# Kernel optimization log

Measured on AMD Instinct MI355X. Metric: run time of the kernel, lower is better.

The kernel has to match this reference:

```python
import jax, jax.numpy as jnp
import numpy as np

BS, L, IMG, RS = 512, 68, 224, 7
R2 = RS * RS
DEPTH_SCALE = 500.0
VALID_RANGE = 90.0
THR = 1e-4


def setup_inputs() -> dict:
    key = jax.random.key(0)
    k1, k2, k3 = jax.random.split(key, 3)
    rel_depth_pred = jax.random.normal(k1, (BS, L, L), dtype=jnp.float32)
    depth = jax.random.uniform(k2, (BS, 1, IMG, IMG), dtype=jnp.float32)
    # landmarks in pixel coords well inside the 224px image so regions are valid
    landmarks = jax.random.uniform(k3, (BS, L, 2), dtype=jnp.float32) * 180.0 + 22.0
    scale_factor = jnp.ones((BS, 2), dtype=jnp.float32)
    bbox = jnp.zeros((BS, 4), dtype=jnp.float32)
    return {"rel_depth_pred": rel_depth_pred, "depth": depth,
            "landmarks": landmarks, "scale_factor": scale_factor, "bbox": bbox}


def _extract_landmark_depth(depth, landmarks, scale_factor, bbox):
    bs, img = depth.shape[0], depth.shape[3]
    # normalized landmark coords in [-1, 1]
    face_lm = (landmarks - bbox[:, None, :2]) * scale_factor[:, None, :] / img * 2.0 - 1.0  # [bs,L,2]
    x = jnp.linspace(-RS / 2.0, RS / 2.0, RS) / img * 2.0
    A, B = jnp.meshgrid(x, x, indexing='ij')          # A[i,j]=x[i], B[i,j]=x[j]
    offsets = jnp.stack([B, A], axis=2)               # torch: stack(meshgrid([x,x])[::-1], dim=2)
    grid = face_lm[:, :, None, None, :] + offsets     # [bs,L,RS,RS,2]
    grid = grid.reshape(bs, L * R2, 2)
    # F.grid_sample mode='nearest', padding='zeros', align_corners=False
    ix = ((grid[..., 0] + 1.0) * img - 1.0) * 0.5
    iy = ((grid[..., 1] + 1.0) * img - 1.0) * 0.5
    xi = jnp.round(ix).astype(jnp.int32)
    yi = jnp.round(iy).astype(jnp.int32)
    valid = (xi >= 0) & (xi < img) & (yi >= 0) & (yi < img)
    xi = jnp.clip(xi, 0, img - 1)
    yi = jnp.clip(yi, 0, img - 1)
    flat = depth.reshape(bs, img * img)
    vals = jnp.take_along_axis(flat, yi * img + xi, axis=1) * valid.astype(depth.dtype)
    regions = vals.reshape(bs, L, R2)
    s = jnp.sort(regions, axis=2)                     # ascending per landmark region
    m = s > THR
    m = m.at[:, :, 0].set(False)                      # torch zeroes index 0 before the diff
    trans = m[:, :, 1:] & ~m[:, :, :-1]               # single 0->1 transition (m is monotone)
    has = jnp.any(trans, axis=2)
    st = jnp.where(has, jnp.argmax(trans, axis=2) + 1, R2 - 1)  # fallback: last index
    med_ind = (st + R2 - 1) // 2                      # ((st + 48)/2).long()
    median = jnp.take_along_axis(s, med_ind[..., None], axis=2)[..., 0]  # [bs,L]
    # torch.median over dim=1: lower median = (L-1)//2-th order statistic
    med_of_med = jnp.sort(median, axis=1)[:, (L - 1) // 2]
    median_mask = jnp.abs(median - med_of_med[:, None]) < VALID_RANGE / DEPTH_SCALE
    return median, median_mask


def reference(rel_depth_pred, depth, landmarks, scale_factor, bbox):
    median, median_mask = _extract_landmark_depth(depth, landmarks, scale_factor, bbox)
    median = median * DEPTH_SCALE
    median_diff = median[:, :, None] - median[:, None, :]            # [bs,L,L]
    fm = median_mask.astype(rel_depth_pred.dtype)
    median_rel_mask = fm[:, :, None] * fm[:, None, :]                # [bs,L,L]
    d = rel_depth_pred - median_diff
    ad = jnp.abs(d)
    loss_ele = jnp.where(ad < 1.0, 0.5 * d * d, ad - 0.5)            # smooth_l1, reduction='none'
    loss = jnp.sum(loss_ele * median_rel_mask) / (jnp.sum(median_rel_mask) + 1e-4)
    return loss, median_diff, median_rel_mask
```

## Files before the change

### kernel.cpp

```cpp
#include <hip/hip_runtime.h>
#include <cfloat>

static constexpr int kBS  = 512;
static constexpr int kL   = 68;
static constexpr int kIMG = 224;
static constexpr int kR2  = 49;
static constexpr int kLL  = kL * kL;
static constexpr int kOutBlk = 256;
static constexpr int kNbx = (kLL + kOutBlk - 1) / kOutBlk;
static constexpr int kNPart = kNbx * kBS;

__device__ __forceinline__ float lin_off(int k) {
  float x;
  if (k == 6) {
    x = 3.5f;
  } else {
    float step = __fdiv_rn((float)k, 6.0f);
    float a = __fmul_rn(-3.5f, __fsub_rn(1.0f, step));
    float b = __fmul_rn(3.5f, step);
    x = __fadd_rn(a, b);
  }
  return __fmul_rn(__fdiv_rn(x, 224.0f), 2.0f);
}

__global__ __launch_bounds__(256) void k_median(
    const float* __restrict__ depth, const float* __restrict__ lmk,
    const float* __restrict__ scale, const float* __restrict__ bbox,
    float* __restrict__ med) {
  int wave = blockIdx.x * 4 + (threadIdx.x >> 6);
  int lane = threadIdx.x & 63;
  if (wave >= kBS * kL) return;
  int b = wave / kL;

  float lmx = lmk[wave * 2 + 0];
  float lmy = lmk[wave * 2 + 1];
  float sx = scale[b * 2 + 0], sy = scale[b * 2 + 1];
  float bx = bbox[b * 4 + 0],  by = bbox[b * 4 + 1];

  float tx = __fsub_rn(lmx, bx);
  tx = __fmul_rn(tx, sx);
  tx = __fdiv_rn(tx, 224.0f);
  tx = __fmul_rn(tx, 2.0f);
  float flmx = __fsub_rn(tx, 1.0f);
  float ty = __fsub_rn(lmy, by);
  ty = __fmul_rn(ty, sy);
  ty = __fdiv_rn(ty, 224.0f);
  ty = __fmul_rn(ty, 2.0f);
  float flmy = __fsub_rn(ty, 1.0f);

  float v = FLT_MAX;
  if (lane < kR2) {
    int i = lane / 7, j = lane - i * 7;
    float gx = __fadd_rn(flmx, lin_off(j));
    float gy = __fadd_rn(flmy, lin_off(i));
    float ix = __fmul_rn(__fsub_rn(__fmul_rn(__fadd_rn(gx, 1.0f), 224.0f), 1.0f), 0.5f);
    float iy = __fmul_rn(__fsub_rn(__fmul_rn(__fadd_rn(gy, 1.0f), 224.0f), 1.0f), 0.5f);
    int xi = (int)rintf(ix);
    int yi = (int)rintf(iy);
    bool valid = (xi >= 0) && (xi < kIMG) && (yi >= 0) && (yi < kIMG);
    int xc = min(max(xi, 0), kIMG - 1);
    int yc = min(max(yi, 0), kIMG - 1);
    float dv = depth[(size_t)b * (kIMG * kIMG) + yc * kIMG + xc];
    v = valid ? dv : 0.0f;
  }

  int cnt = 0, rank = 0;
  for (int j = 0; j < kR2; ++j) {
    float vj = __shfl(v, j, 64);
    cnt += (vj <= 1e-4f) ? 1 : 0;
    rank += ((vj < v) || (vj == v && j < lane)) ? 1 : 0;
  }
  int st = min(max(cnt, 1), kR2 - 1);
  int k = (st + kR2 - 1) >> 1;
  unsigned long long sel = __ballot(lane < kR2 && rank == k);
  int src = __ffsll(sel) - 1;
  float m = __shfl(v, src, 64);
  if (lane == 0) med[wave] = m;
}

__global__ __launch_bounds__(128) void k_mask(
    const float* __restrict__ med, float* __restrict__ m500,
    float* __restrict__ fm) {
  __shared__ float s[kL];
  __shared__ float mom_s;
  int b = blockIdx.x;
  int t = threadIdx.x;
  if (t < kL) s[t] = med[b * kL + t];
  __syncthreads();
  if (t < kL) {
    float v = s[t];
    int rank = 0;
    for (int j = 0; j < kL; ++j) {
      float vj = s[j];
      rank += ((vj < v) || (vj == v && j < t)) ? 1 : 0;
    }
    if (rank == (kL - 1) / 2) mom_s = v;
  }
  __syncthreads();
  if (t < kL) {
    float v = s[t];
    float diff = fabsf(__fsub_rn(v, mom_s));
    fm[b * kL + t] = (diff < 0.18f) ? 1.0f : 0.0f;
    m500[b * kL + t] = __fmul_rn(v, 500.0f);
  }
}

__global__ __launch_bounds__(256) void k_out(
    const float* __restrict__ rdp, const float* __restrict__ m500,
    const float* __restrict__ fm, float* __restrict__ out_diff,
    float* __restrict__ out_mask, double* __restrict__ part) {
  int b = blockIdx.y;
  int t = blockIdx.x * blockDim.x + threadIdx.x;
  double pn = 0.0, pd = 0.0;
  if (t < kLL) {
    int i = t / kL, j = t - i * kL;
    float mi = m500[b * kL + i];
    float mj = m500[b * kL + j];
    float diff = __fsub_rn(mi, mj);
    float mv = __fmul_rn(fm[b * kL + i], fm[b * kL + j]);
    size_t idx = (size_t)b * kLL + t;
    out_diff[idx] = diff;
    out_mask[idx] = mv;
    float d = __fsub_rn(rdp[idx], diff);
    float ad = fabsf(d);
    float le = (ad < 1.0f) ? __fmul_rn(__fmul_rn(0.5f, d), d)
                           : __fsub_rn(ad, 0.5f);
    pn = (double)__fmul_rn(le, mv);
    pd = (double)mv;
  }
  for (int off = 32; off > 0; off >>= 1) {
    pn += __shfl_down(pn, off, 64);
    pd += __shfl_down(pd, off, 64);
  }
  __shared__ double sn[4], sd[4];
  int w = threadIdx.x >> 6;
  if ((threadIdx.x & 63) == 0) { sn[w] = pn; sd[w] = pd; }
  __syncthreads();
  if (threadIdx.x == 0) {
    double tn = sn[0] + sn[1] + sn[2] + sn[3];
    double td = sd[0] + sd[1] + sd[2] + sd[3];
    int pb = blockIdx.y * gridDim.x + blockIdx.x;
    part[2 * pb + 0] = tn;
    part[2 * pb + 1] = td;
  }
}

__global__ __launch_bounds__(256) void k_final(
    const double* __restrict__ part, float* __restrict__ out0) {
  double pn = 0.0, pd = 0.0;
  for (int i = threadIdx.x; i < kNPart; i += 256) {
    pn += part[2 * i + 0];
    pd += part[2 * i + 1];
  }
  for (int off = 32; off > 0; off >>= 1) {
    pn += __shfl_down(pn, off, 64);
    pd += __shfl_down(pd, off, 64);
  }
  __shared__ double sn[4], sd[4];
  int w = threadIdx.x >> 6;
  if ((threadIdx.x & 63) == 0) { sn[w] = pn; sd[w] = pd; }
  __syncthreads();
  if (threadIdx.x == 0) {
    double tn = sn[0] + sn[1] + sn[2] + sn[3];
    double td = sd[0] + sd[1] + sd[2] + sd[3];
    out0[0] = (float)(tn / (td + 1e-4));
  }
}

extern "C" void kernel_launch(void* const* d_in, const int* in_sizes, int n_in,
                              void* d_out, int out_size, void* d_ws, size_t ws_size,
                              hipStream_t stream) {
  const float* rdp   = (const float*)d_in[0];
  const float* depth = (const float*)d_in[1];
  const float* lmk   = (const float*)d_in[2];
  const float* scale = (const float*)d_in[3];
  const float* bbox  = (const float*)d_in[4];

  float* out = (float*)d_out;
  float* out_diff = out + 1;
  float* out_mask = out + 1 + (size_t)kBS * kLL;

  char* ws = (char*)d_ws;
  const size_t medBytes = (size_t)kBS * kL * sizeof(float);
  float*  med   = (float*)(ws);
  float*  m500  = (float*)(ws + medBytes);
  float*  fm    = (float*)(ws + 2 * medBytes);
  double* part  = (double*)(ws + 3 * medBytes);

  int nWaves = kBS * kL;
  int nBlk1 = (nWaves + 3) / 4;
  k_median<<<dim3(nBlk1), dim3(256), 0, stream>>>(depth, lmk, scale, bbox, med);
  k_mask<<<dim3(kBS), dim3(128), 0, stream>>>(med, m500, fm);
  k_out<<<dim3(kNbx, kBS), dim3(kOutBlk), 0, stream>>>(rdp, m500, fm, out_diff,
                                                       out_mask, part);
  k_final<<<dim3(1), dim3(256), 0, stream>>>(part, out);
}
```

Measured before the change: 197.8 us.

## Fuse median and mask kernels, fold final reduction into output kernel

Merges the per-landmark median and per-batch mask kernels into one block per batch. Each of the 68 regions is handled by 8 lanes doing the rank selection over register arrays. The final reduction moves into the output kernel as a last-block-done atomic counter, and the output kernel stages medians in shared memory with 4 blocks per batch. Together this drops two kernel launches and their round trips through global memory, at the cost of a threadfence/atomic protocol and a counter reset done inside the first kernel.

```diff
diff --git a/kernel.cpp b/kernel.cpp
--- a/kernel.cpp
+++ b/kernel.cpp
@@ -6,164 +6,184 @@
 static constexpr int kIMG = 224;
 static constexpr int kR2  = 49;
 static constexpr int kLL  = kL * kL;
-static constexpr int kOutBlk = 256;
-static constexpr int kNbx = (kLL + kOutBlk - 1) / kOutBlk;
-static constexpr int kNPart = kNbx * kBS;
-
-__device__ __forceinline__ float lin_off(int k) {
-  float x;
-  if (k == 6) {
-    x = 3.5f;
-  } else {
-    float step = __fdiv_rn((float)k, 6.0f);
-    float a = __fmul_rn(-3.5f, __fsub_rn(1.0f, step));
-    float b = __fmul_rn(3.5f, step);
-    x = __fadd_rn(a, b);
-  }
+
+__device__ __forceinline__ float lin_off_rt(int k) {
+  float step = __fdiv_rn((float)k, 6.0f);
+  float a = __fmul_rn(-3.5f, __fsub_rn(1.0f, step));
+  float bb = __fmul_rn(3.5f, step);
+  float x = __fadd_rn(a, bb);
   return __fmul_rn(__fdiv_rn(x, 224.0f), 2.0f);
 }
 
-__global__ __launch_bounds__(256) void k_median(
+__global__ __launch_bounds__(576) void k_med_mask(
     const float* __restrict__ depth, const float* __restrict__ lmk,
     const float* __restrict__ scale, const float* __restrict__ bbox,
-    float* __restrict__ med) {
-  int wave = blockIdx.x * 4 + (threadIdx.x >> 6);
-  int lane = threadIdx.x & 63;
-  if (wave >= kBS * kL) return;
-  int b = wave / kL;
-
-  float lmx = lmk[wave * 2 + 0];
-  float lmy = lmk[wave * 2 + 1];
+    float* __restrict__ m500, float* __restrict__ fm,
+    unsigned long long* __restrict__ ctl) {
+  __shared__ float med_s[kL];
+  __shared__ float mom_s;
+  int b = blockIdx.x;
+  int tid = threadIdx.x;
+  int wave = tid >> 6, lane = tid & 63;
+  int g = lane >> 3, r = lane & 7;
+  int lreg = wave * 8 + g;
+  int rr = min(lreg, kL - 1);
+
+  float lmx = lmk[(b * kL + rr) * 2 + 0];
+  float lmy = lmk[(b * kL + rr) * 2 + 1];
   float sx = scale[b * 2 + 0], sy = scale[b * 2 + 1];
   float bx = bbox[b * 4 + 0],  by = bbox[b * 4 + 1];
 
   float tx = __fsub_rn(lmx, bx);
-  tx = __fmul_rn(tx, sx);
-  tx = __fdiv_rn(tx, 224.0f);
-  tx = __fmul_rn(tx, 2.0f);
+  tx = __fmul_rn(tx, sx); tx = __fdiv_rn(tx, 224.0f); tx = __fmul_rn(tx, 2.0f);
   float flmx = __fsub_rn(tx, 1.0f);
   float ty = __fsub_rn(lmy, by);
-  ty = __fmul_rn(ty, sy);
-  ty = __fdiv_rn(ty, 224.0f);
-  ty = __fmul_rn(ty, 2.0f);
+  ty = __fmul_rn(ty, sy); ty = __fdiv_rn(ty, 224.0f); ty = __fmul_rn(ty, 2.0f);
   float flmy = __fsub_rn(ty, 1.0f);
 
-  float v = FLT_MAX;
-  if (lane < kR2) {
-    int i = lane / 7, j = lane - i * 7;
-    float gx = __fadd_rn(flmx, lin_off(j));
-    float gy = __fadd_rn(flmy, lin_off(i));
-    float ix = __fmul_rn(__fsub_rn(__fmul_rn(__fadd_rn(gx, 1.0f), 224.0f), 1.0f), 0.5f);
-    float iy = __fmul_rn(__fsub_rn(__fmul_rn(__fadd_rn(gy, 1.0f), 224.0f), 1.0f), 0.5f);
-    int xi = (int)rintf(ix);
-    int yi = (int)rintf(iy);
-    bool valid = (xi >= 0) && (xi < kIMG) && (yi >= 0) && (yi < kIMG);
-    int xc = min(max(xi, 0), kIMG - 1);
-    int yc = min(max(yi, 0), kIMG - 1);
-    float dv = depth[(size_t)b * (kIMG * kIMG) + yc * kIMG + xc];
-    v = valid ? dv : 0.0f;
-  }
-
-  int cnt = 0, rank = 0;
-  for (int j = 0; j < kR2; ++j) {
-    float vj = __shfl(v, j, 64);
-    cnt += (vj <= 1e-4f) ? 1 : 0;
-    rank += ((vj < v) || (vj == v && j < lane)) ? 1 : 0;
+  const float* img = depth + (size_t)b * (kIMG * kIMG);
+  float v[7];
+#pragma unroll
+  for (int s = 0; s < 7; ++s) {
+    int idx = r + 8 * s;
+    if (idx < kR2) {
+      unsigned i7 = (unsigned)idx / 7u;
+      int j7 = idx - (int)i7 * 7;
+      float gx = __fadd_rn(flmx, lin_off_rt(j7));
+      float gy = __fadd_rn(flmy, lin_off_rt((int)i7));
+      float ix = __fmul_rn(__fsub_rn(__fmul_rn(__fadd_rn(gx, 1.0f), 224.0f), 1.0f), 0.5f);
+      float iy = __fmul_rn(__fsub_rn(__fmul_rn(__fadd_rn(gy, 1.0f), 224.0f), 1.0f), 0.5f);
+      int xi = (int)rintf(ix), yi = (int)rintf(iy);
+      bool val = (xi >= 0) && (xi < kIMG) && (yi >= 0) && (yi < kIMG);
+      int xc = min(max(xi, 0), kIMG - 1), yc = min(max(yi, 0), kIMG - 1);
+      float dv = img[yc * kIMG + xc];
+      v[s] = val ? dv : 0.0f;
+    } else {
+      v[s] = FLT_MAX;
+    }
+  }
+
+  int rank[7] = {0, 0, 0, 0, 0, 0, 0};
+  int cnt = 0;
+  int gb = lane & 56;
+#pragma unroll
+  for (int t = 0; t < 8; ++t) {
+    float w[7];
+#pragma unroll
+    for (int s = 0; s < 7; ++s) w[s] = __shfl(v[s], gb + t, 64);
+#pragma unroll
+    for (int s = 0; s < 7; ++s) {
+      const int widx = t + 8 * s;
+      if (widx < kR2) cnt += (w[s] <= 1e-4f) ? 1 : 0;
+#pragma unroll
+      for (int m = 0; m < 7; ++m) {
+        bool less = (w[s] < v[m]) || ((w[s] == v[m]) && (widx < r + 8 * m));
+        rank[m] += less ? 1 : 0;
+      }
+    }
   }
   int st = min(max(cnt, 1), kR2 - 1);
-  int k = (st + kR2 - 1) >> 1;
-  unsigned long long sel = __ballot(lane < kR2 && rank == k);
-  int src = __ffsll(sel) - 1;
-  float m = __shfl(v, src, 64);
-  if (lane == 0) med[wave] = m;
-}
-
-__global__ __launch_bounds__(128) void k_mask(
-    const float* __restrict__ med, float* __restrict__ m500,
-    float* __restrict__ fm) {
-  __shared__ float s[kL];
-  __shared__ float mom_s;
-  int b = blockIdx.x;
-  int t = threadIdx.x;
-  if (t < kL) s[t] = med[b * kL + t];
-  __syncthreads();
-  if (t < kL) {
-    float v = s[t];
-    int rank = 0;
+  int kk = (st + kR2 - 1) >> 1;
+  float sel = 0.0f;
+#pragma unroll
+  for (int m = 0; m < 7; ++m)
+    if ((r + 8 * m) < kR2 && rank[m] == kk) sel = v[m];
+  int sb = __float_as_int(sel);
+  sb |= __shfl_xor(sb, 1, 64);
+  sb |= __shfl_xor(sb, 2, 64);
+  sb |= __shfl_xor(sb, 4, 64);
+  if (r == 0 && lreg < kL) med_s[lreg] = __int_as_float(sb);
+  if (b == 0 && tid >= 128 && tid < 144) ctl[tid - 128] = 0ull;
+  __syncthreads();
+
+  if (tid < kL) {
+    float mv = med_s[tid];
+    int rnk = 0;
     for (int j = 0; j < kL; ++j) {
-      float vj = s[j];
-      rank += ((vj < v) || (vj == v && j < t)) ? 1 : 0;
-    }
-    if (rank == (kL - 1) / 2) mom_s = v;
-  }
-  __syncthreads();
-  if (t < kL) {
-    float v = s[t];
-    float diff = fabsf(__fsub_rn(v, mom_s));
-    fm[b * kL + t] = (diff < 0.18f) ? 1.0f : 0.0f;
-    m500[b * kL + t] = __fmul_rn(v, 500.0f);
+      float vj = med_s[j];
+      rnk += ((vj < mv) || (vj == mv && j < tid)) ? 1 : 0;
+    }
+    if (rnk == (kL - 1) / 2) mom_s = mv;
+  }
+  __syncthreads();
+  if (tid < kL) {
+    float mv = med_s[tid];
+    float diff = fabsf(__fsub_rn(mv, mom_s));
+    fm[b * kL + tid] = (diff < 0.18f) ? 1.0f : 0.0f;
+    m500[b * kL + tid] = __fmul_rn(mv, 500.0f);
   }
 }
 
 __global__ __launch_bounds__(256) void k_out(
     const float* __restrict__ rdp, const float* __restrict__ m500,
     const float* __restrict__ fm, float* __restrict__ out_diff,
-    float* __restrict__ out_mask, double* __restrict__ part) {
-  int b = blockIdx.y;
-  int t = blockIdx.x * blockDim.x + threadIdx.x;
+    float* __restrict__ out_mask, float* __restrict__ out0,
+    unsigned long long* __restrict__ ctl, char* __restrict__ part) {
+  __shared__ float s_m[kL], s_f[kL];
+  __shared__ double sn[4], sd[4];
+  __shared__ int lastFlag;
+  int b = blockIdx.y, bx = blockIdx.x, t = threadIdx.x;
+  if (t < kL) { s_m[t] = m500[b * kL + t]; s_f[t] = fm[b * kL + t]; }
+  __syncthreads();
+
+  int base = bx * 1156;
   double pn = 0.0, pd = 0.0;
-  if (t < kLL) {
-    int i = t / kL, j = t - i * kL;
-    float mi = m500[b * kL + i];
-    float mj = m500[b * kL + j];
-    float diff = __fsub_rn(mi, mj);
-    float mv = __fmul_rn(fm[b * kL + i], fm[b * kL + j]);
-    size_t idx = (size_t)b * kLL + t;
-    out_diff[idx] = diff;
-    out_mask[idx] = mv;
-    float d = __fsub_rn(rdp[idx], diff);
-    float ad = fabsf(d);
-    float le = (ad < 1.0f) ? __fmul_rn(__fmul_rn(0.5f, d), d)
-                           : __fsub_rn(ad, 0.5f);
-    pn = (double)__fmul_rn(le, mv);
-    pd = (double)mv;
+#pragma unroll
+  for (int k2 = 0; k2 < 5; ++k2) {
+    int e = base + t + k2 * 256;
+    if (e < base + 1156) {
+      unsigned i = (unsigned)e / 68u;
+      int j = e - (int)i * 68;
+      float mi = s_m[i], mj = s_m[j];
+      float diff = __fsub_rn(mi, mj);
+      float mv = __fmul_rn(s_f[i], s_f[j]);
+      size_t idx = (size_t)b * kLL + e;
+      out_diff[idx] = diff;
+      out_mask[idx] = mv;
+      float d = __fsub_rn(rdp[idx], diff);
+      float ad = fabsf(d);
+      float le = (ad < 1.0f) ? __fmul_rn(__fmul_rn(0.5f, d), d)
+                             : __fsub_rn(ad, 0.5f);
+      pn += (double)__fmul_rn(le, mv);
+      pd += (double)mv;
+    }
   }
   for (int off = 32; off > 0; off >>= 1) {
     pn += __shfl_down(pn, off, 64);
     pd += __shfl_down(pd, off, 64);
   }
-  __shared__ double sn[4], sd[4];
-  int w = threadIdx.x >> 6;
-  if ((threadIdx.x & 63) == 0) { sn[w] = pn; sd[w] = pd; }
-  __syncthreads();
-  if (threadIdx.x == 0) {
+  int w = t >> 6;
+  if ((t & 63) == 0) { sn[w] = pn; sd[w] = pd; }
+  __syncthreads();
+  int blkid = b * 4 + bx;
+  if (t == 0) {
     double tn = sn[0] + sn[1] + sn[2] + sn[3];
     double td = sd[0] + sd[1] + sd[2] + sd[3];
-    int pb = blockIdx.y * gridDim.x + blockIdx.x;
-    part[2 * pb + 0] = tn;
-    part[2 * pb + 1] = td;
-  }
-}
-
-__global__ __launch_bounds__(256) void k_final(
-    const double* __restrict__ part, float* __restrict__ out0) {
-  double pn = 0.0, pd = 0.0;
-  for (int i = threadIdx.x; i < kNPart; i += 256) {
-    pn += part[2 * i + 0];
-    pd += part[2 * i + 1];
-  }
-  for (int off = 32; off > 0; off >>= 1) {
-    pn += __shfl_down(pn, off, 64);
-    pd += __shfl_down(pd, off, 64);
-  }
-  __shared__ double sn[4], sd[4];
-  int w = threadIdx.x >> 6;
-  if ((threadIdx.x & 63) == 0) { sn[w] = pn; sd[w] = pd; }
-  __syncthreads();
-  if (threadIdx.x == 0) {
-    double tn = sn[0] + sn[1] + sn[2] + sn[3];
-    double td = sd[0] + sd[1] + sd[2] + sd[3];
-    out0[0] = (float)(tn / (td + 1e-4));
+    double* pe = (double*)(part + (size_t)blkid * 128);
+    pe[0] = tn; pe[1] = td;
+    __threadfence();
+    unsigned old = atomicAdd((unsigned*)ctl, 1u);
+    lastFlag = (old == 2047u);
+  }
+  __syncthreads();
+  if (lastFlag) {
+    __threadfence();
+    double n = 0.0, dd = 0.0;
+    for (int i = t; i < 2048; i += 256) {
+      double* pe = (double*)(part + (size_t)i * 128);
+      n += pe[0]; dd += pe[1];
+    }
+    for (int off = 32; off > 0; off >>= 1) {
+      n += __shfl_down(n, off, 64);
+      dd += __shfl_down(dd, off, 64);
+    }
+    if ((t & 63) == 0) { sn[t >> 6] = n; sd[t >> 6] = dd; }
+    __syncthreads();
+    if (t == 0) {
+      double tn = sn[0] + sn[1] + sn[2] + sn[3];
+      double td = sd[0] + sd[1] + sd[2] + sd[3];
+      out0[0] = (float)(tn / (td + 1e-4));
+    }
   }
 }
 
@@ -181,17 +201,13 @@
   float* out_mask = out + 1 + (size_t)kBS * kLL;
 
   char* ws = (char*)d_ws;
-  const size_t medBytes = (size_t)kBS * kL * sizeof(float);
-  float*  med   = (float*)(ws);
-  float*  m500  = (float*)(ws + medBytes);
-  float*  fm    = (float*)(ws + 2 * medBytes);
-  double* part  = (double*)(ws + 3 * medBytes);
-
-  int nWaves = kBS * kL;
-  int nBlk1 = (nWaves + 3) / 4;
-  k_median<<<dim3(nBlk1), dim3(256), 0, stream>>>(depth, lmk, scale, bbox, med);
-  k_mask<<<dim3(kBS), dim3(128), 0, stream>>>(med, m500, fm);
-  k_out<<<dim3(kNbx, kBS), dim3(kOutBlk), 0, stream>>>(rdp, m500, fm, out_diff,
-                                                       out_mask, part);
-  k_final<<<dim3(1), dim3(256), 0, stream>>>(part, out);
-}
+  unsigned long long* ctl = (unsigned long long*)ws;
+  float* m500 = (float*)(ws + 128);
+  float* fm   = (float*)(ws + 128 + 139264);
+  char*  part = ws + 128 + 2 * 139264;
+
+  k_med_mask<<<dim3(kBS), dim3(576), 0, stream>>>(depth, lmk, scale, bbox,
+                                                  m500, fm, ctl);
+  k_out<<<dim3(4, kBS), dim3(256), 0, stream>>>(rdp, m500, fm, out_diff,
+                                                out_mask, out, ctl, part);
+}
```

Result: slower. 291.0 us (+47.1%).

## Fuse final reduction into output kernel via last-block atomic counter

Applied to the files above, without the earlier changes.

Removes the separate final reduction kernel: each output block writes its partial sums, bumps an atomic counter, and the last block to finish reduces all partials and writes the loss. The counter is reset inside the median kernel. The output kernel now flattens the batch into a 1D grid with two elements per thread and reads rel_depth_pred as float2. Median*500 and the mask flag are packed into one float2 array so each lookup is a single load. This saves a kernel launch and removes the tail blocks' idle lanes, in exchange for an atomic and fences plus unaligned scalar stores to the outputs, which start one float past the buffer base.

```diff
diff --git a/kernel.cpp b/kernel.cpp
--- a/kernel.cpp
+++ b/kernel.cpp
@@ -6,27 +6,22 @@
 static constexpr int kIMG = 224;
 static constexpr int kR2  = 49;
 static constexpr int kLL  = kL * kL;
-static constexpr int kOutBlk = 256;
-static constexpr int kNbx = (kLL + kOutBlk - 1) / kOutBlk;
-static constexpr int kNPart = kNbx * kBS;
+static constexpr int kPairsTotal = kBS * kLL / 2;
+static constexpr int kOutBlocks = kPairsTotal / 256;
 
 __device__ __forceinline__ float lin_off(int k) {
-  float x;
-  if (k == 6) {
-    x = 3.5f;
-  } else {
-    float step = __fdiv_rn((float)k, 6.0f);
-    float a = __fmul_rn(-3.5f, __fsub_rn(1.0f, step));
-    float b = __fmul_rn(3.5f, step);
-    x = __fadd_rn(a, b);
-  }
+  float step = __fdiv_rn((float)k, 6.0f);
+  float a = __fmul_rn(-3.5f, __fsub_rn(1.0f, step));
+  float b = __fmul_rn(3.5f, step);
+  float x = __fadd_rn(a, b);
   return __fmul_rn(__fdiv_rn(x, 224.0f), 2.0f);
 }
 
 __global__ __launch_bounds__(256) void k_median(
     const float* __restrict__ depth, const float* __restrict__ lmk,
     const float* __restrict__ scale, const float* __restrict__ bbox,
-    float* __restrict__ med) {
+    float* __restrict__ med, unsigned* __restrict__ ctl) {
+  if (blockIdx.x == 0 && threadIdx.x == 0) ctl[0] = 0u;
   int wave = blockIdx.x * 4 + (threadIdx.x >> 6);
   int lane = threadIdx.x & 63;
   if (wave >= kBS * kL) return;
@@ -38,14 +33,10 @@
   float bx = bbox[b * 4 + 0],  by = bbox[b * 4 + 1];
 
   float tx = __fsub_rn(lmx, bx);
-  tx = __fmul_rn(tx, sx);
-  tx = __fdiv_rn(tx, 224.0f);
-  tx = __fmul_rn(tx, 2.0f);
+  tx = __fmul_rn(tx, sx); tx = __fdiv_rn(tx, 224.0f); tx = __fmul_rn(tx, 2.0f);
   float flmx = __fsub_rn(tx, 1.0f);
   float ty = __fsub_rn(lmy, by);
-  ty = __fmul_rn(ty, sy);
-  ty = __fdiv_rn(ty, 224.0f);
-  ty = __fmul_rn(ty, 2.0f);
+  ty = __fmul_rn(ty, sy); ty = __fdiv_rn(ty, 224.0f); ty = __fmul_rn(ty, 2.0f);
   float flmy = __fsub_rn(ty, 1.0f);
 
   float v = FLT_MAX;
@@ -55,11 +46,9 @@
     float gy = __fadd_rn(flmy, lin_off(i));
     float ix = __fmul_rn(__fsub_rn(__fmul_rn(__fadd_rn(gx, 1.0f), 224.0f), 1.0f), 0.5f);
     float iy = __fmul_rn(__fsub_rn(__fmul_rn(__fadd_rn(gy, 1.0f), 224.0f), 1.0f), 0.5f);
-    int xi = (int)rintf(ix);
-    int yi = (int)rintf(iy);
+    int xi = (int)rintf(ix), yi = (int)rintf(iy);
     bool valid = (xi >= 0) && (xi < kIMG) && (yi >= 0) && (yi < kIMG);
-    int xc = min(max(xi, 0), kIMG - 1);
-    int yc = min(max(yi, 0), kIMG - 1);
+    int xc = min(max(xi, 0), kIMG - 1), yc = min(max(yi, 0), kIMG - 1);
     float dv = depth[(size_t)b * (kIMG * kIMG) + yc * kIMG + xc];
     v = valid ? dv : 0.0f;
   }
@@ -79,12 +68,10 @@
 }
 
 __global__ __launch_bounds__(128) void k_mask(
-    const float* __restrict__ med, float* __restrict__ m500,
-    float* __restrict__ fm) {
+    const float* __restrict__ med, float2* __restrict__ mf) {
   __shared__ float s[kL];
   __shared__ float mom_s;
-  int b = blockIdx.x;
-  int t = threadIdx.x;
+  int b = blockIdx.x, t = threadIdx.x;
   if (t < kL) s[t] = med[b * kL + t];
   __syncthreads();
   if (t < kL) {
@@ -100,70 +87,83 @@
   if (t < kL) {
     float v = s[t];
     float diff = fabsf(__fsub_rn(v, mom_s));
-    fm[b * kL + t] = (diff < 0.18f) ? 1.0f : 0.0f;
-    m500[b * kL + t] = __fmul_rn(v, 500.0f);
+    float2 o;
+    o.x = __fmul_rn(v, 500.0f);
+    o.y = (diff < 0.18f) ? 1.0f : 0.0f;
+    mf[b * kL + t] = o;
   }
 }
 
 __global__ __launch_bounds__(256) void k_out(
-    const float* __restrict__ rdp, const float* __restrict__ m500,
-    const float* __restrict__ fm, float* __restrict__ out_diff,
-    float* __restrict__ out_mask, double* __restrict__ part) {
-  int b = blockIdx.y;
-  int t = blockIdx.x * blockDim.x + threadIdx.x;
-  double pn = 0.0, pd = 0.0;
-  if (t < kLL) {
-    int i = t / kL, j = t - i * kL;
-    float mi = m500[b * kL + i];
-    float mj = m500[b * kL + j];
-    float diff = __fsub_rn(mi, mj);
-    float mv = __fmul_rn(fm[b * kL + i], fm[b * kL + j]);
-    size_t idx = (size_t)b * kLL + t;
-    out_diff[idx] = diff;
-    out_mask[idx] = mv;
-    float d = __fsub_rn(rdp[idx], diff);
-    float ad = fabsf(d);
-    float le = (ad < 1.0f) ? __fmul_rn(__fmul_rn(0.5f, d), d)
-                           : __fsub_rn(ad, 0.5f);
-    pn = (double)__fmul_rn(le, mv);
-    pd = (double)mv;
-  }
+    const float* __restrict__ rdp, const float2* __restrict__ mf,
+    float* __restrict__ out_diff, float* __restrict__ out_mask,
+    float* __restrict__ out0, unsigned* __restrict__ ctl,
+    double* __restrict__ part) {
+  __shared__ double sn[4], sd[4];
+  __shared__ int lastFlag;
+  int t = blockIdx.x * 256 + threadIdx.x;
+  int e = t * 2;
+  unsigned b = (unsigned)e / (unsigned)kLL;
+  int r = e - (int)b * kLL;
+  unsigned i0 = (unsigned)r / (unsigned)kL;
+  int j0 = r - (int)i0 * kL;
+  unsigned i1 = (j0 == kL - 1) ? i0 + 1 : i0;
+  int j1 = (j0 == kL - 1) ? 0 : j0 + 1;
+
+  const float2* mfb = mf + b * kL;
+  float2 a0 = mfb[i0], a1 = mfb[i1];
+  float2 c0 = mfb[j0], c1 = mfb[j1];
+  float2 rp = ((const float2*)rdp)[t];
+
+  float diff0 = __fsub_rn(a0.x, c0.x);
+  float diff1 = __fsub_rn(a1.x, c1.x);
+  float mv0 = __fmul_rn(a0.y, c0.y);
+  float mv1 = __fmul_rn(a1.y, c1.y);
+  out_diff[e] = diff0; out_diff[e + 1] = diff1;
+  out_mask[e] = mv0;   out_mask[e + 1] = mv1;
+
+  float d0 = __fsub_rn(rp.x, diff0), d1 = __fsub_rn(rp.y, diff1);
+  float ad0 = fabsf(d0), ad1 = fabsf(d1);
+  float le0 = (ad0 < 1.0f) ? __fmul_rn(__fmul_rn(0.5f, d0), d0) : __fsub_rn(ad0, 0.5f);
+  float le1 = (ad1 < 1.0f) ? __fmul_rn(__fmul_rn(0.5f, d1), d1) : __fsub_rn(ad1, 0.5f);
+  double pn = (double)__fmul_rn(le0, mv0) + (double)__fmul_rn(le1, mv1);
+  double pd = (double)mv0 + (double)mv1;
+
   for (int off = 32; off > 0; off >>= 1) {
     pn += __shfl_down(pn, off, 64);
     pd += __shfl_down(pd, off, 64);
   }
-  __shared__ double sn[4], sd[4];
   int w = threadIdx.x >> 6;
   if ((threadIdx.x & 63) == 0) { sn[w] = pn; sd[w] = pd; }
   __syncthreads();
   if (threadIdx.x == 0) {
     double tn = sn[0] + sn[1] + sn[2] + sn[3];
     double td = sd[0] + sd[1] + sd[2] + sd[3];
-    int pb = blockIdx.y * gridDim.x + blockIdx.x;
-    part[2 * pb + 0] = tn;
-    part[2 * pb + 1] = td;
+    part[2 * blockIdx.x + 0] = tn;
+    part[2 * blockIdx.x + 1] = td;
+    __threadfence();
+    unsigned old = atomicAdd(ctl, 1u);
+    lastFlag = (old == (unsigned)(kOutBlocks - 1));
   }
-}
-
-__global__ __launch_bounds__(256) void k_final(
-    const double* __restrict__ part, float* __restrict__ out0) {
-  double pn = 0.0, pd = 0.0;
-  for (int i = threadIdx.x; i < kNPart; i += 256) {
-    pn += part[2 * i + 0];
-    pd += part[2 * i + 1];
-  }
-  for (int off = 32; off > 0; off >>= 1) {
-    pn += __shfl_down(pn, off, 64);
-    pd += __shfl_down(pd, off, 64);
-  }
-  __shared__ double sn[4], sd[4];
-  int w = threadIdx.x >> 6;
-  if ((threadIdx.x & 63) == 0) { sn[w] = pn; sd[w] = pd; }
   __syncthreads();
-  if (threadIdx.x == 0) {
-    double tn = sn[0] + sn[1] + sn[2] + sn[3];
-    double td = sd[0] + sd[1] + sd[2] + sd[3];
-    out0[0] = (float)(tn / (td + 1e-4));
+  if (lastFlag) {
+    __threadfence();
+    double n = 0.0, dd = 0.0;
+    for (int i = threadIdx.x; i < kOutBlocks; i += 256) {
+      n += part[2 * i + 0];
+      dd += part[2 * i + 1];
+    }
+    for (int off = 32; off > 0; off >>= 1) {
+      n += __shfl_down(n, off, 64);
+      dd += __shfl_down(dd, off, 64);
+    }
+    if ((threadIdx.x & 63) == 0) { sn[threadIdx.x >> 6] = n; sd[threadIdx.x >> 6] = dd; }
+    __syncthreads();
+    if (threadIdx.x == 0) {
+      double tn = sn[0] + sn[1] + sn[2] + sn[3];
+      double td = sd[0] + sd[1] + sd[2] + sd[3];
+      out0[0] = (float)(tn / (td + 1e-4));
+    }
   }
 }
 
@@ -181,17 +181,15 @@
   float* out_mask = out + 1 + (size_t)kBS * kLL;
 
   char* ws = (char*)d_ws;
-  const size_t medBytes = (size_t)kBS * kL * sizeof(float);
-  float*  med   = (float*)(ws);
-  float*  m500  = (float*)(ws + medBytes);
-  float*  fm    = (float*)(ws + 2 * medBytes);
-  double* part  = (double*)(ws + 3 * medBytes);
+  unsigned* ctl = (unsigned*)ws;
+  float*  med  = (float*)(ws + 128);
+  float2* mf   = (float2*)(ws + 128 + 139264);
+  double* part = (double*)(ws + 128 + 139264 + 278528);
 
   int nWaves = kBS * kL;
   int nBlk1 = (nWaves + 3) / 4;
-  k_median<<<dim3(nBlk1), dim3(256), 0, stream>>>(depth, lmk, scale, bbox, med);
-  k_mask<<<dim3(kBS), dim3(128), 0, stream>>>(med, m500, fm);
-  k_out<<<dim3(kNbx, kBS), dim3(kOutBlk), 0, stream>>>(rdp, m500, fm, out_diff,
-                                                       out_mask, part);
-  k_final<<<dim3(1), dim3(256), 0, stream>>>(part, out);
+  k_median<<<dim3(nBlk1), dim3(256), 0, stream>>>(depth, lmk, scale, bbox, med, ctl);
+  k_mask<<<dim3(kBS), dim3(128), 0, stream>>>(med, mf);
+  k_out<<<dim3(kOutBlocks), dim3(256), 0, stream>>>(rdp, mf, out_diff, out_mask,
+                                                    out, ctl, part);
 }
```

Measured after the change: 334.4 us. 1.69x slower.
